# Kernel optimization log

Measured on AMD Instinct MI355X. Metric: run time of the kernel, lower is better.

Reference implementation:

```python
import jax, jax.numpy as jnp
import numpy as np
import math

B, S, HID = 4, 2048, 1024
N_HEADS, HEAD_DIM = 16, 64
LOGITS_CAP = 30.0
EPS = 1e-6

def setup_inputs() -> dict:
    key = jax.random.key(0)
    ks = jax.random.split(key, 8)
    sd = 1.0 / math.sqrt(HID)
    return {
        "hidden_states": jax.random.normal(ks[0], (B, S, HID), dtype=jnp.float32),
        "attention_mask": jnp.zeros((B, 1, 1, S), dtype=jnp.float32),
        "Wq": jax.random.normal(ks[1], (HID, HID), dtype=jnp.float32) * sd,
        "bq": jnp.zeros((HID,), dtype=jnp.float32),
        "Wk": jax.random.normal(ks[2], (HID, HID), dtype=jnp.float32) * sd,
        "bk": jnp.zeros((HID,), dtype=jnp.float32),
        "Wv": jax.random.normal(ks[3], (HID, HID), dtype=jnp.float32) * sd,
        "bv": jnp.zeros((HID,), dtype=jnp.float32),
    }

def _heads(x):
    # [B,S,HID] -> [B,N_HEADS,S,HEAD_DIM]
    return x.reshape(B, S, N_HEADS, HEAD_DIM).transpose(0, 2, 1, 3)

def reference(hidden_states, attention_mask, Wq, bq, Wk, bk, Wv, bv):
    # QKV projections (torch Linear: x @ W.T + b)
    q = _heads(jnp.einsum('bsh,oh->bso', hidden_states, Wq) + bq)
    k = _heads(jnp.einsum('bsh,oh->bso', hidden_states, Wk) + bk)
    v = _heads(jnp.einsum('bsh,oh->bso', hidden_states, Wv) + bv)
    # raw scores [B,H,S,S], scaled (softmax_2RELU path uses 1/sqrt(d))
    scores = jnp.einsum('bnqd,bnkd->bnqk', q, k) / math.sqrt(HEAD_DIM)
    scores = scores + attention_mask
    # tanh logit soft-capping
    scores = jnp.tanh(scores / LOGITS_CAP) * LOGITS_CAP
    # softmax_2RELU: relu(x) / (sum relu(x) + eps)
    r = jax.nn.relu(scores)
    probs = r / (jnp.sum(r, axis=-1, keepdims=True) + EPS)
    # context [B,H,S,D] -> [B,S,HID]
    ctx = jnp.einsum('bnqk,bnkd->bnqd', probs, v)
    return ctx.transpose(0, 2, 1, 3).reshape(B, S, HID)
```

## Files before the change

kernel.cpp:

```cpp
#include <hip/hip_runtime.h>
#include <hip/hip_bf16.h>

#define B_    4
#define S_    2048
#define HID_  1024
#define NH_   16
#define HD_   64
#define C3_  (-3.7037037037e-4f)
#define C5_  (1.64609053498e-7f)

typedef __attribute__((ext_vector_type(8))) short short8;
typedef __attribute__((ext_vector_type(4))) float float4v;

static __device__ __forceinline__ unsigned short f2bf(float f) {
    unsigned u = __builtin_bit_cast(unsigned, f);
    u = (u + 0x7fffu + ((u >> 16) & 1u)) >> 16;
    return (unsigned short)u;
}

__global__ void convert_all(const float* __restrict__ h,
                            const float* __restrict__ wq,
                            const float* __restrict__ wk,
                            const float* __restrict__ wv,
                            unsigned short* __restrict__ hb,
                            unsigned short* __restrict__ wqb,
                            unsigned short* __restrict__ wkb,
                            unsigned short* __restrict__ wvb) {
    const int which = blockIdx.y;
    const float* src = (which == 0) ? h : (which == 1) ? wq : (which == 2) ? wk : wv;
    unsigned short* dst = (which == 0) ? hb : (which == 1) ? wqb : (which == 2) ? wkb : wvb;
    const int n4 = ((which == 0) ? (B_ * S_ * HID_) : (HID_ * HID_)) / 4;
    int i = blockIdx.x * blockDim.x + threadIdx.x;
    const int st = gridDim.x * blockDim.x;
    for (; i < n4; i += st) {
        float4 v = ((const float4*)src)[i];
        ushort4 o;
        o.x = f2bf(v.x); o.y = f2bf(v.y); o.z = f2bf(v.z); o.w = f2bf(v.w);
        ((ushort4*)dst)[i] = o;
    }
}

__global__ __launch_bounds__(256) void qkv_gemm(
    const unsigned short* __restrict__ hb,
    const unsigned short* __restrict__ wqb,
    const unsigned short* __restrict__ wkb,
    const unsigned short* __restrict__ wvb,
    const float* __restrict__ bq,
    const float* __restrict__ bk,
    const float* __restrict__ bv,
    unsigned short* __restrict__ q_ws,
    unsigned short* __restrict__ k_ws,
    unsigned short* __restrict__ vt_ws) {
    const int z = blockIdx.z;
    const unsigned short* wgt = (z == 0) ? wqb : ((z == 1) ? wkb : wvb);
    const float* bias = (z == 0) ? bq : ((z == 1) ? bk : bv);
    const int n0 = blockIdx.x * 128;
    const int m0 = blockIdx.y * 128;

    __shared__ unsigned short As[128 * 64];
    __shared__ unsigned short Bs[128 * 64];

    const int tid = threadIdx.x;
    const int lane = tid & 63;
    const int w = tid >> 6;
    const int wm = w >> 1, wn = w & 1;
    const int l15 = lane & 15;
    const int g = lane >> 4;

    const int srow = lane >> 3;
    const int schunk = (lane & 7) ^ srow;
    const int scol = schunk * 8;

    const int xm = (l15 & 7) << 4;
    const int roff0 = l15 * 128 + ((g * 16) ^ xm);
    const int roff1 = l15 * 128 + ((g * 16 + 64) ^ xm);

    float4v acc[4][4] = {};

    for (int k0 = 0; k0 < HID_; k0 += 64) {
#pragma unroll
        for (int j = 0; j < 4; j++) {
            const int row = j * 32 + w * 8 + srow;
            const unsigned short* gA = &hb[(size_t)(m0 + row) * HID_ + k0 + scol];
            const unsigned short* gB = &wgt[(size_t)(n0 + row) * HID_ + k0 + scol];
            __builtin_amdgcn_global_load_lds(
                (const __attribute__((address_space(1))) unsigned int*)gA,
                (__attribute__((address_space(3))) unsigned int*)((char*)As + (j * 32 + w * 8) * 128),
                16, 0, 0);
            __builtin_amdgcn_global_load_lds(
                (const __attribute__((address_space(1))) unsigned int*)gB,
                (__attribute__((address_space(3))) unsigned int*)((char*)Bs + (j * 32 + w * 8) * 128),
                16, 0, 0);
        }
        __syncthreads();

        short8 af0[4], af1[4], bf0[4], bf1[4];
#pragma unroll
        for (int mf = 0; mf < 4; mf++) {
            const char* ab = (const char*)As + (wm * 64 + mf * 16) * 128;
            af0[mf] = *(const short8*)(ab + roff0);
            af1[mf] = *(const short8*)(ab + roff1);
        }
#pragma unroll
        for (int nf = 0; nf < 4; nf++) {
            const char* bb = (const char*)Bs + (wn * 64 + nf * 16) * 128;
            bf0[nf] = *(const short8*)(bb + roff0);
            bf1[nf] = *(const short8*)(bb + roff1);
        }
#pragma unroll
        for (int mf = 0; mf < 4; mf++)
#pragma unroll
            for (int nf = 0; nf < 4; nf++) {
                acc[mf][nf] = __builtin_amdgcn_mfma_f32_16x16x32_bf16(af0[mf], bf0[nf], acc[mf][nf], 0, 0, 0);
                acc[mf][nf] = __builtin_amdgcn_mfma_f32_16x16x32_bf16(af1[mf], bf1[nf], acc[mf][nf], 0, 0, 0);
            }
        __syncthreads();
    }

#pragma unroll
    for (int mf = 0; mf < 4; mf++)
#pragma unroll
        for (int nf = 0; nf < 4; nf++) {
            const int o = n0 + wn * 64 + nf * 16 + l15;
            const float bb = bias[o];
            const int h = o >> 6, d = o & 63;
#pragma unroll
            for (int r = 0; r < 4; r++) {
                const int m = m0 + wm * 64 + mf * 16 + g * 4 + r;
                const int b = m >> 11, s = m & 2047;
                float val = acc[mf][nf][r] + bb;
                if (z == 0) val *= 0.125f;
                const unsigned short bfv = f2bf(val);
                if (z == 2)
                    vt_ws[(((size_t)(b * NH_ + h)) * HD_ + d) * S_ + s] = bfv;
                else if (z == 0)
                    q_ws[(((size_t)(b * NH_ + h)) * S_ + s) * HD_ + d] = bfv;
                else
                    k_ws[(((size_t)(b * NH_ + h)) * S_ + s) * HD_ + d] = bfv;
            }
        }
}

__global__ __launch_bounds__(256) void attn_kernel(
    const unsigned short* __restrict__ q_ws,
    const unsigned short* __restrict__ k_ws,
    const unsigned short* __restrict__ vt_ws,
    const float* __restrict__ mask,
    float* __restrict__ out) {
    const int qt = blockIdx.x;
    const int bh = blockIdx.y;
    const int b = bh >> 4, h = bh & 15;
    const unsigned short* qp = q_ws + (size_t)bh * S_ * HD_;
    const unsigned short* kp = k_ws + (size_t)bh * S_ * HD_;
    const unsigned short* vp = vt_ws + (size_t)bh * HD_ * S_;
    const float* mp = mask + (size_t)b * S_;

    __shared__ unsigned short Kl[2][64 * 64];
    __shared__ unsigned short Vl[2][64 * 64];
    __shared__ unsigned short Pl[4][32][72];

    const int tid = threadIdx.x, lane = tid & 63, w = tid >> 6;
    const int l15 = lane & 15;
    const int g = lane >> 4;
    const int kk = g * 8;

    const int srow = lane >> 3;
    const int schunk = (lane & 7) ^ srow;
    const int scol = schunk * 8;

    const int xm = (l15 & 7) << 4;
    const int roff0 = l15 * 128 + ((g * 16) ^ xm);
    const int roff1 = l15 * 128 + ((g * 16 + 64) ^ xm);

    short8 qf[2][2];
#pragma unroll
    for (int t = 0; t < 2; t++) {
        const int qrow = qt * 128 + w * 32 + t * 16 + l15;
        qf[t][0] = *(const short8*)&qp[(size_t)qrow * HD_ + kk];
        qf[t][1] = *(const short8*)&qp[(size_t)qrow * HD_ + 32 + kk];
    }

    const short8 ones = {0x3F80, 0x3F80, 0x3F80, 0x3F80, 0x3F80, 0x3F80, 0x3F80, 0x3F80};

    float4v ctx[2][4] = {};
    float4v ctxS[2] = {};

    auto stage = [&](int kt, int buf) {
#pragma unroll
        for (int j = 0; j < 2; j++) {
            const unsigned short* gK =
                &kp[(size_t)(kt * 64 + j * 32 + w * 8 + srow) * HD_ + scol];
            __builtin_amdgcn_global_load_lds(
                (const __attribute__((address_space(1))) unsigned int*)gK,
                (__attribute__((address_space(3))) unsigned int*)((char*)&Kl[buf][0] + (j * 32 + w * 8) * 128),
                16, 0, 0);
            const unsigned short* gV =
                &vp[(size_t)(j * 32 + w * 8 + srow) * S_ + kt * 64 + scol];
            __builtin_amdgcn_global_load_lds(
                (const __attribute__((address_space(1))) unsigned int*)gV,
                (__attribute__((address_space(3))) unsigned int*)((char*)&Vl[buf][0] + (j * 32 + w * 8) * 128),
                16, 0, 0);
        }
    };

    stage(0, 0);
    asm volatile("s_waitcnt vmcnt(0)" ::: "memory");
    __builtin_amdgcn_s_barrier();

    int cur = 0;
    for (int kt = 0; kt < 32; kt++) {
        if (kt < 31) stage(kt + 1, cur ^ 1);

        float mv[4];
#pragma unroll
        for (int n = 0; n < 4; n++) mv[n] = mp[kt * 64 + n * 16 + l15];

        const char* kb = (const char*)&Kl[cur][0];
        float4v sfr[2][4];
#pragma unroll
        for (int n = 0; n < 4; n++) {
            short8 kf0 = *(const short8*)(kb + n * 2048 + roff0);
            short8 kf1 = *(const short8*)(kb + n * 2048 + roff1);
#pragma unroll
            for (int t = 0; t < 2; t++) {
                float4v a = {};
                a = __builtin_amdgcn_mfma_f32_16x16x32_bf16(qf[t][0], kf0, a, 0, 0, 0);
                a = __builtin_amdgcn_mfma_f32_16x16x32_bf16(qf[t][1], kf1, a, 0, 0, 0);
                sfr[t][n] = a;
            }
        }

#pragma unroll
        for (int t = 0; t < 2; t++)
#pragma unroll
            for (int n = 0; n < 4; n++) {
                float rl[4];
#pragma unroll
                for (int r = 0; r < 4; r++) {
                    float s = sfr[t][n][r] + mv[n];
                    float u = s * s;
                    float su = s * u;
                    float tt = __builtin_fmaf(u, C5_, C3_);
                    float p = __builtin_fmaf(su, tt, s);
                    rl[r] = fmaxf(p, 0.0f);
                }
                unsigned int d01, d23;
                asm("v_cvt_pk_bf16_f32 %0, %1, %2" : "=v"(d01) : "v"(rl[0]), "v"(rl[1]));
                asm("v_cvt_pk_bf16_f32 %0, %1, %2" : "=v"(d23) : "v"(rl[2]), "v"(rl[3]));
                unsigned short* pr = &Pl[w][t * 16 + g * 4][n * 16 + l15];
                pr[0]   = (unsigned short)d01;
                pr[72]  = (unsigned short)(d01 >> 16);
                pr[144] = (unsigned short)d23;
                pr[216] = (unsigned short)(d23 >> 16);
            }

        short8 pf[2][2];
#pragma unroll
        for (int t = 0; t < 2; t++) {
            pf[t][0] = *(const short8*)&Pl[w][t * 16 + l15][kk];
            pf[t][1] = *(const short8*)&Pl[w][t * 16 + l15][32 + kk];
            ctxS[t] = __builtin_amdgcn_mfma_f32_16x16x32_bf16(pf[t][0], ones, ctxS[t], 0, 0, 0);
            ctxS[t] = __builtin_amdgcn_mfma_f32_16x16x32_bf16(pf[t][1], ones, ctxS[t], 0, 0, 0);
        }
        const char* vb = (const char*)&Vl[cur][0];
#pragma unroll
        for (int n = 0; n < 4; n++) {
            short8 vf0 = *(const short8*)(vb + n * 2048 + roff0);
            short8 vf1 = *(const short8*)(vb + n * 2048 + roff1);
#pragma unroll
            for (int t = 0; t < 2; t++) {
                ctx[t][n] = __builtin_amdgcn_mfma_f32_16x16x32_bf16(pf[t][0], vf0, ctx[t][n], 0, 0, 0);
                ctx[t][n] = __builtin_amdgcn_mfma_f32_16x16x32_bf16(pf[t][1], vf1, ctx[t][n], 0, 0, 0);
            }
        }

        asm volatile("s_waitcnt vmcnt(0)" ::: "memory");
        __builtin_amdgcn_s_barrier();
        cur ^= 1;
    }

#pragma unroll
    for (int t = 0; t < 2; t++) {
        float rinv[4];
#pragma unroll
        for (int r = 0; r < 4; r++)
            rinv[r] = __builtin_amdgcn_rcpf(ctxS[t][r] + 1e-6f);
#pragma unroll
        for (int n = 0; n < 4; n++) {
            const int d = n * 16 + l15;
#pragma unroll
            for (int r = 0; r < 4; r++) {
                const int qrow = qt * 128 + w * 32 + t * 16 + g * 4 + r;
                out[((size_t)b * S_ + qrow) * HID_ + h * HD_ + d] = ctx[t][n][r] * rinv[r];
            }
        }
    }
}

extern "C" void kernel_launch(void* const* d_in, const int* in_sizes, int n_in,
                              void* d_out, int out_size, void* d_ws, size_t ws_size,
                              hipStream_t stream) {
    const float* hidden = (const float*)d_in[0];
    const float* mask   = (const float*)d_in[1];
    const float* Wq     = (const float*)d_in[2];
    const float* bq     = (const float*)d_in[3];
    const float* Wk     = (const float*)d_in[4];
    const float* bk     = (const float*)d_in[5];
    const float* Wv     = (const float*)d_in[6];
    const float* bv     = (const float*)d_in[7];
    float* out = (float*)d_out;

    char* ws = (char*)d_ws;
    const size_t HB_BYTES = (size_t)B_ * S_ * HID_ * 2;
    const size_t W_BYTES  = (size_t)HID_ * HID_ * 2;
    const size_t QKV_BYTES = (size_t)B_ * NH_ * S_ * HD_ * 2;

    unsigned short* hb    = (unsigned short*)(ws);
    unsigned short* wqb   = (unsigned short*)(ws + HB_BYTES);
    unsigned short* wkb   = (unsigned short*)(ws + HB_BYTES + W_BYTES);
    unsigned short* wvb   = (unsigned short*)(ws + HB_BYTES + 2 * W_BYTES);
    unsigned short* q_wsp = (unsigned short*)(ws + HB_BYTES + 3 * W_BYTES);
    unsigned short* k_wsp = (unsigned short*)(ws + HB_BYTES + 3 * W_BYTES + QKV_BYTES);
    unsigned short* vt_wsp = (unsigned short*)(ws + HB_BYTES + 3 * W_BYTES + 2 * QKV_BYTES);

    dim3 cgrid(1024, 4);
    convert_all<<<cgrid, 256, 0, stream>>>(hidden, Wq, Wk, Wv, hb, wqb, wkb, wvb);

    dim3 ggrid(HID_ / 128, (B_ * S_) / 128, 3);
    qkv_gemm<<<ggrid, 256, 0, stream>>>(hb, wqb, wkb, wvb, bq, bk, bv,
                                        q_wsp, k_wsp, vt_wsp);

    dim3 agrid(S_ / 128, B_ * NH_);
    attn_kernel<<<agrid, 256, 0, stream>>>(q_wsp, k_wsp, vt_wsp, mask, out);
}
```

Baseline: 305.2 us.

## Fold Q scale into weights, transpose V GEMM output, double attention block size

The Q scaling of 1/8 is applied when Wq is converted to bf16, and the bias is scaled in the epilogue instead of multiplying each output. For the V projection the GEMM swaps operands so each lane's output index runs along the sequence axis, which makes the transposed V stores more contiguous. The attention kernel now uses 512-thread blocks covering 256 query rows, so each K/V tile staged in LDS serves twice as many queries, with one load per thread per stage. The larger blocks use more LDS and registers per block, which may lower occupancy, and the pre-scaled Q weights round differently in bf16.

```diff
diff --git a/kernel.cpp b/kernel.cpp
--- a/kernel.cpp
+++ b/kernel.cpp
@@ -29,13 +29,14 @@
     const int which = blockIdx.y;
     const float* src = (which == 0) ? h : (which == 1) ? wq : (which == 2) ? wk : wv;
     unsigned short* dst = (which == 0) ? hb : (which == 1) ? wqb : (which == 2) ? wkb : wvb;
+    const float sc = (which == 1) ? 0.125f : 1.0f;
     const int n4 = ((which == 0) ? (B_ * S_ * HID_) : (HID_ * HID_)) / 4;
     int i = blockIdx.x * blockDim.x + threadIdx.x;
     const int st = gridDim.x * blockDim.x;
     for (; i < n4; i += st) {
         float4 v = ((const float4*)src)[i];
         ushort4 o;
-        o.x = f2bf(v.x); o.y = f2bf(v.y); o.z = f2bf(v.z); o.w = f2bf(v.w);
+        o.x = f2bf(v.x * sc); o.y = f2bf(v.y * sc); o.z = f2bf(v.z * sc); o.w = f2bf(v.w * sc);
         ((ushort4*)dst)[i] = o;
     }
 }
@@ -54,8 +55,11 @@
     const int z = blockIdx.z;
     const unsigned short* wgt = (z == 0) ? wqb : ((z == 1) ? wkb : wvb);
     const float* bias = (z == 0) ? bq : ((z == 1) ? bk : bv);
-    const int n0 = blockIdx.x * 128;
-    const int m0 = blockIdx.y * 128;
+    const bool zswap = (z == 2);
+    const int arow0 = zswap ? blockIdx.x * 128 : blockIdx.y * 128;
+    const int brow0 = zswap ? blockIdx.y * 128 : blockIdx.x * 128;
+    const unsigned short* At = zswap ? wgt : hb;
+    const unsigned short* Bt = zswap ? hb : wgt;
 
     __shared__ unsigned short As[128 * 64];
     __shared__ unsigned short Bs[128 * 64];
@@ -81,8 +85,8 @@
 #pragma unroll
         for (int j = 0; j < 4; j++) {
             const int row = j * 32 + w * 8 + srow;
-            const unsigned short* gA = &hb[(size_t)(m0 + row) * HID_ + k0 + scol];
-            const unsigned short* gB = &wgt[(size_t)(n0 + row) * HID_ + k0 + scol];
+            const unsigned short* gA = &At[(size_t)(arow0 + row) * HID_ + k0 + scol];
+            const unsigned short* gB = &Bt[(size_t)(brow0 + row) * HID_ + k0 + scol];
             __builtin_amdgcn_global_load_lds(
                 (const __attribute__((address_space(1))) unsigned int*)gA,
                 (__attribute__((address_space(3))) unsigned int*)((char*)As + (j * 32 + w * 8) * 128),
@@ -117,31 +121,49 @@
         __syncthreads();
     }
 
-#pragma unroll
-    for (int mf = 0; mf < 4; mf++)
-#pragma unroll
-        for (int nf = 0; nf < 4; nf++) {
-            const int o = n0 + wn * 64 + nf * 16 + l15;
-            const float bb = bias[o];
-            const int h = o >> 6, d = o & 63;
-#pragma unroll
-            for (int r = 0; r < 4; r++) {
-                const int m = m0 + wm * 64 + mf * 16 + g * 4 + r;
+    if (!zswap) {
+#pragma unroll
+        for (int mf = 0; mf < 4; mf++)
+#pragma unroll
+            for (int nf = 0; nf < 4; nf++) {
+                const int o = brow0 + wn * 64 + nf * 16 + l15;
+                const float bb = bias[o] * ((z == 0) ? 0.125f : 1.0f);
+                const int h = o >> 6, d = o & 63;
+#pragma unroll
+                for (int r = 0; r < 4; r++) {
+                    const int m = arow0 + wm * 64 + mf * 16 + g * 4 + r;
+                    const int b = m >> 11, s = m & 2047;
+                    const unsigned short bfv = f2bf(acc[mf][nf][r] + bb);
+                    if (z == 0)
+                        q_ws[(((size_t)(b * NH_ + h)) * S_ + s) * HD_ + d] = bfv;
+                    else
+                        k_ws[(((size_t)(b * NH_ + h)) * S_ + s) * HD_ + d] = bfv;
+                }
+            }
+    } else {
+#pragma unroll
+        for (int mf = 0; mf < 4; mf++) {
+            const int obase = arow0 + wm * 64 + mf * 16 + g * 4;
+            float bbr[4];
+#pragma unroll
+            for (int r = 0; r < 4; r++) bbr[r] = bias[obase + r];
+#pragma unroll
+            for (int nf = 0; nf < 4; nf++) {
+                const int m = brow0 + wn * 64 + nf * 16 + l15;
                 const int b = m >> 11, s = m & 2047;
-                float val = acc[mf][nf][r] + bb;
-                if (z == 0) val *= 0.125f;
-                const unsigned short bfv = f2bf(val);
-                if (z == 2)
-                    vt_ws[(((size_t)(b * NH_ + h)) * HD_ + d) * S_ + s] = bfv;
-                else if (z == 0)
-                    q_ws[(((size_t)(b * NH_ + h)) * S_ + s) * HD_ + d] = bfv;
-                else
-                    k_ws[(((size_t)(b * NH_ + h)) * S_ + s) * HD_ + d] = bfv;
-            }
-        }
-}
-
-__global__ __launch_bounds__(256) void attn_kernel(
+#pragma unroll
+                for (int r = 0; r < 4; r++) {
+                    const int o = obase + r;
+                    const int h = o >> 6, d = o & 63;
+                    vt_ws[(((size_t)(b * NH_ + h)) * HD_ + d) * S_ + s] =
+                        f2bf(acc[mf][nf][r] + bbr[r]);
+                }
+            }
+        }
+    }
+}
+
+__global__ __launch_bounds__(512, 4) void attn_kernel(
     const unsigned short* __restrict__ q_ws,
     const unsigned short* __restrict__ k_ws,
     const unsigned short* __restrict__ vt_ws,
@@ -157,7 +179,7 @@
 
     __shared__ unsigned short Kl[2][64 * 64];
     __shared__ unsigned short Vl[2][64 * 64];
-    __shared__ unsigned short Pl[4][32][72];
+    __shared__ unsigned short Pl[8][32][72];
 
     const int tid = threadIdx.x, lane = tid & 63, w = tid >> 6;
     const int l15 = lane & 15;
@@ -175,7 +197,7 @@
     short8 qf[2][2];
 #pragma unroll
     for (int t = 0; t < 2; t++) {
-        const int qrow = qt * 128 + w * 32 + t * 16 + l15;
+        const int qrow = qt * 256 + w * 32 + t * 16 + l15;
         qf[t][0] = *(const short8*)&qp[(size_t)qrow * HD_ + kk];
         qf[t][1] = *(const short8*)&qp[(size_t)qrow * HD_ + 32 + kk];
     }
@@ -186,21 +208,18 @@
     float4v ctxS[2] = {};
 
     auto stage = [&](int kt, int buf) {
-#pragma unroll
-        for (int j = 0; j < 2; j++) {
-            const unsigned short* gK =
-                &kp[(size_t)(kt * 64 + j * 32 + w * 8 + srow) * HD_ + scol];
-            __builtin_amdgcn_global_load_lds(
-                (const __attribute__((address_space(1))) unsigned int*)gK,
-                (__attribute__((address_space(3))) unsigned int*)((char*)&Kl[buf][0] + (j * 32 + w * 8) * 128),
-                16, 0, 0);
-            const unsigned short* gV =
-                &vp[(size_t)(j * 32 + w * 8 + srow) * S_ + kt * 64 + scol];
-            __builtin_amdgcn_global_load_lds(
-                (const __attribute__((address_space(1))) unsigned int*)gV,
-                (__attribute__((address_space(3))) unsigned int*)((char*)&Vl[buf][0] + (j * 32 + w * 8) * 128),
-                16, 0, 0);
-        }
+        const unsigned short* gK =
+            &kp[(size_t)(kt * 64 + w * 8 + srow) * HD_ + scol];
+        __builtin_amdgcn_global_load_lds(
+            (const __attribute__((address_space(1))) unsigned int*)gK,
+            (__attribute__((address_space(3))) unsigned int*)((char*)&Kl[buf][0] + (w * 8) * 128),
+            16, 0, 0);
+        const unsigned short* gV =
+            &vp[(size_t)(w * 8 + srow) * S_ + kt * 64 + scol];
+        __builtin_amdgcn_global_load_lds(
+            (const __attribute__((address_space(1))) unsigned int*)gV,
+            (__attribute__((address_space(3))) unsigned int*)((char*)&Vl[buf][0] + (w * 8) * 128),
+            16, 0, 0);
     };
 
     stage(0, 0);
@@ -290,7 +309,7 @@
             const int d = n * 16 + l15;
 #pragma unroll
             for (int r = 0; r < 4; r++) {
-                const int qrow = qt * 128 + w * 32 + t * 16 + g * 4 + r;
+                const int qrow = qt * 256 + w * 32 + t * 16 + g * 4 + r;
                 out[((size_t)b * S_ + qrow) * HID_ + h * HD_ + d] = ctx[t][n][r] * rinv[r];
             }
         }
@@ -330,6 +349,6 @@
     qkv_gemm<<<ggrid, 256, 0, stream>>>(hb, wqb, wkb, wvb, bq, bk, bv,
                                         q_wsp, k_wsp, vt_wsp);
 
-    dim3 agrid(S_ / 128, B_ * NH_);
-    attn_kernel<<<agrid, 256, 0, stream>>>(q_wsp, k_wsp, vt_wsp, mask, out);
-}
+    dim3 agrid(S_ / 256, B_ * NH_);
+    attn_kernel<<<agrid, 512, 0, stream>>>(q_wsp, k_wsp, vt_wsp, mask, out);
+}
```

After: 265.8 us. 12.9% less time.
